# Optimization experiments

Hardware: AMD Instinct MI355X
Metric: run time of the kernel (lower is better)

## Reference

```python
import jax, jax.numpy as jnp
import numpy as np

D = 256  # input_dim
B = 2048

def setup_inputs() -> dict:
    key = jax.random.key(0)
    ks = jax.random.split(key, 6)
    x = jax.random.normal(ks[0], (B, D), dtype=jnp.float32)
    offsets = jax.random.normal(ks[1], (D,), dtype=jnp.float32)
    coeff0 = jax.random.normal(ks[2], (), dtype=jnp.float32)
    coeff1 = jax.random.normal(ks[3], (D,), dtype=jnp.float32)
    coeff2 = jax.random.normal(ks[4], (D, D), dtype=jnp.float32)
    coeff3 = jax.random.normal(ks[5], (D, D, D), dtype=jnp.float32)
    return {"x": x, "offsets": offsets, "coeff0": coeff0, "coeff1": coeff1,
            "coeff2": coeff2, "coeff3": coeff3}

def reference(x, offsets, coeff0, coeff1, coeff2, coeff3):
    # Truncated Taylor series around learned offsets: out[b] = c0 + sum_i <coeff_i, rel^{\otimes i}>[b]
    rel = x - offsets  # (B, D)
    out = coeff0  # scalar, broadcasts to (B,)
    for c in (coeff1, coeff2, coeff3):
        # contract one mode of the rank-i coefficient with rel at a time
        t = jnp.einsum('...d,bd->b...', c, rel)  # (B, D^{i-1})
        while t.ndim > 1:
            t = jnp.einsum('b...d,bd->b...', t, rel)
        out = out + t  # (B,)
    return out
```

## Files before the change

### kernel.cpp

```cpp
#include <hip/hip_runtime.h>
#include <hip/hip_bf16.h>

#define DD 256
#define BB 2048
#define BM 128
#define BN 32
#define NTILE 512
#define NSTAGE (BB / BN)

typedef __bf16 bf16x8 __attribute__((ext_vector_type(8)));
typedef float  f32x4  __attribute__((ext_vector_type(4)));

#define AS1 __attribute__((address_space(1)))
#define AS3 __attribute__((address_space(3)))

__device__ __forceinline__ unsigned short f2bf(float f) {
    unsigned int u = __float_as_uint(f);
    return (unsigned short)((u + 0x7FFFu + ((u >> 16) & 1u)) >> 16);
}
__device__ __forceinline__ float bf2f(unsigned short s) {
    return __uint_as_float(((unsigned int)s) << 16);
}
__device__ __forceinline__ void async_cp16(const void* g, void* l) {
    __builtin_amdgcn_global_load_lds((const AS1 unsigned int*)g,
                                     (AS3 unsigned int*)l, 16, 0, 0);
}

__global__ void prep_all(const float* __restrict__ x, const float* __restrict__ offsets,
                         const float* __restrict__ c0, const float* __restrict__ c1,
                         unsigned short* __restrict__ rel_bf16, float* __restrict__ out) {
    const int tid = threadIdx.x, wave = tid >> 6, lane = tid & 63;
    const float4 o4  = *(const float4*)(offsets + lane * 4);
    const float4 c14 = *(const float4*)(c1 + lane * 4);
#pragma unroll
    for (int i = 0; i < 2; ++i) {
        const int b = blockIdx.x * 8 + wave * 2 + i;
        const float4 x4 = *(const float4*)(x + (size_t)b * DD + lane * 4);
        float4 r;
        r.x = x4.x - o4.x; r.y = x4.y - o4.y; r.z = x4.z - o4.z; r.w = x4.w - o4.w;
        ushort4 rb;
        rb.x = f2bf(r.x); rb.y = f2bf(r.y); rb.z = f2bf(r.z); rb.w = f2bf(r.w);
        *(ushort4*)(rel_bf16 + (size_t)b * DD + lane * 4) = rb;
        float s = r.x * c14.x + r.y * c14.y + r.z * c14.z + r.w * c14.w;
        s += __shfl_xor(s, 1);  s += __shfl_xor(s, 2);  s += __shfl_xor(s, 4);
        s += __shfl_xor(s, 8);  s += __shfl_xor(s, 16); s += __shfl_xor(s, 32);
        if (lane == 0) out[b] = c0[0] + s;
    }
}

__global__ __launch_bounds__(512, 4) void taylor3(
    const float* __restrict__ c3, const float* __restrict__ c2,
    const unsigned short* __restrict__ rel_bf16, float* __restrict__ partial)
{
    __shared__ unsigned short Bs[2][BN * DD];
    __shared__ unsigned short relIbf[BB];
    __shared__ __align__(16) float c2row[BM];
    __shared__ float colsum[2][8][BN];

    const int bidx  = blockIdx.x;
    const int i_t   = bidx >> 1;
    const int jbase = (bidx & 1) << 7;
    const int tid  = threadIdx.x;
    const int wave = tid >> 6;
    const int lane = tid & 63;
    const int wm = wave & 1, wk = wave >> 1;
    const int lrow = lane & 15, quad = lane >> 4;

#pragma unroll
    for (int k = 0; k < 4; ++k) {
        const int b = tid + k * 512;
        relIbf[b] = rel_bf16[(size_t)b * DD + i_t];
    }
    if (tid < BM) c2row[tid] = c2[i_t * DD + jbase + tid];

    bf16x8 afr[2][4];
    {
#pragma unroll
        for (int mt = 0; mt < 4; ++mt) {
            const int j = jbase + wm * 64 + mt * 16 + lrow;
            const float* p = c3 + ((size_t)i_t * DD + j) * DD + wk * 64 + quad * 8;
#pragma unroll
            for (int ks = 0; ks < 2; ++ks) {
                const float4 f0 = *(const float4*)(p + ks * 32);
                const float4 f1 = *(const float4*)(p + ks * 32 + 4);
                union { unsigned short u[8]; bf16x8 v; } cv;
                cv.u[0] = f2bf(f0.x); cv.u[1] = f2bf(f0.y);
                cv.u[2] = f2bf(f0.z); cv.u[3] = f2bf(f0.w);
                cv.u[4] = f2bf(f1.x); cv.u[5] = f2bf(f1.y);
                cv.u[6] = f2bf(f1.z); cv.u[7] = f2bf(f1.w);
                afr[ks][mt] = cv.v;
            }
        }
    }

    auto stage = [&](int nb, int buf) {
        const int b0 = nb * BN;
#pragma unroll
        for (int c = 0; c < 2; ++c) {
            const int r0 = c * 16 + wave * 2;
            const int row = r0 + (lane >> 5);
            const int g = (lane & 31) ^ (row & 7);
            const unsigned short* src = rel_bf16 + (size_t)(b0 + row) * DD + g * 8;
            async_cp16(src, &Bs[buf][r0 * DD]);
        }
    };

    auto body = [&](int nb, int cur) {
        const int b0 = nb * BN;
        __syncthreads();
        if (nb + 1 < NSTAGE) stage(nb + 1, cur ^ 1);

        if (nb > 0 && wave == 0 && lane < BN) {
            const int pb0 = b0 - BN;
            float v = colsum[cur ^ 1][0][lane];
#pragma unroll
            for (int w = 1; w < 8; ++w) v += colsum[cur ^ 1][w][lane];
            partial[(size_t)bidx * BB + pb0 + lane] = bf2f(relIbf[pb0 + lane]) * v;
        }

        f32x4 acc[4][2];
        __builtin_amdgcn_s_setprio(1);
        {
            bf16x8 bfr[2];
#pragma unroll
            for (int nt = 0; nt < 2; ++nt) {
                const int col = nt * 16 + lrow;
                const int glog = wk * 8 + quad;
                const int g = glog ^ (col & 7);
                bfr[nt] = *(const bf16x8*)(&Bs[cur][col * DD + g * 8]);
            }
            const f32x4 z4 = (f32x4){0.f, 0.f, 0.f, 0.f};
#pragma unroll
            for (int mt = 0; mt < 4; ++mt)
#pragma unroll
                for (int nt = 0; nt < 2; ++nt)
                    acc[mt][nt] = __builtin_amdgcn_mfma_f32_16x16x32_bf16(
                        afr[0][mt], bfr[nt], z4, 0, 0, 0);
        }
        {
            bf16x8 bfr[2];
#pragma unroll
            for (int nt = 0; nt < 2; ++nt) {
                const int col = nt * 16 + lrow;
                const int glog = wk * 8 + 4 + quad;
                const int g = glog ^ (col & 7);
                bfr[nt] = *(const bf16x8*)(&Bs[cur][col * DD + g * 8]);
            }
#pragma unroll
            for (int mt = 0; mt < 4; ++mt)
#pragma unroll
                for (int nt = 0; nt < 2; ++nt)
                    acc[mt][nt] = __builtin_amdgcn_mfma_f32_16x16x32_bf16(
                        afr[1][mt], bfr[nt], acc[mt][nt], 0, 0, 0);
        }
        __builtin_amdgcn_s_setprio(0);

        float sv[2];
#pragma unroll
        for (int nt = 0; nt < 2; ++nt) {
            const int col = nt * 16 + lrow;
            float s0 = 0.f, s1 = 0.f;
#pragma unroll
            for (int mt = 0; mt < 4; ++mt) {
                const int el = wm * 64 + mt * 16 + quad * 4;
                const int e  = jbase + el;
                const int g  = (e >> 3) ^ (col & 7);
                const ushort4 rj = *(const ushort4*)(&Bs[cur][col * DD + g * 8 + (e & 7)]);
                f32x4 a = acc[mt][nt];
                if (wk == 0) {
                    const float4 c2r = *(const float4*)(&c2row[el]);
                    a[0] += c2r.x; a[1] += c2r.y; a[2] += c2r.z; a[3] += c2r.w;
                }
                float& sa = (mt & 1) ? s1 : s0;
                sa = fmaf(a[0], bf2f(rj.x), sa);
                sa = fmaf(a[1], bf2f(rj.y), sa);
                sa = fmaf(a[2], bf2f(rj.z), sa);
                sa = fmaf(a[3], bf2f(rj.w), sa);
            }
            float s = s0 + s1;
            s += __shfl_xor(s, 16, 64);
            s += __shfl_xor(s, 32, 64);
            sv[nt] = s;
        }
        if (lane < 32)
            colsum[cur][wave][lane] = (lane & 16) ? sv[1] : sv[0];
    };

    stage(0, 0);
    for (int nb = 0; nb < NSTAGE; nb += 2) {
        body(nb, 0);
        body(nb + 1, 1);
    }

    __syncthreads();
    if (wave == 0 && lane < BN) {
        const int pb0 = BB - BN;
        float v = colsum[1][0][lane];
#pragma unroll
        for (int w = 1; w < 8; ++w) v += colsum[1][w][lane];
        partial[(size_t)bidx * BB + pb0 + lane] = bf2f(relIbf[pb0 + lane]) * v;
    }
}

__global__ void reduce_partial(const float* __restrict__ partial, float* __restrict__ out) {
    __shared__ f32x4 red[256];
    const int t = threadIdx.x;
    const int g = blockIdx.x * 4 + (t & 3);
    const int slice = t >> 2;
    f32x4 s = (f32x4){0.f, 0.f, 0.f, 0.f};
    for (int r = slice * 8; r < slice * 8 + 8; ++r)
        s += *(const f32x4*)(partial + (size_t)r * BB + g * 4);
    red[t] = s; __syncthreads();
    if (t < 128) red[t] += red[t + 128]; __syncthreads();
    if (t < 64)  red[t] += red[t + 64];  __syncthreads();
    if (t < 32)  red[t] += red[t + 32];  __syncthreads();
    if (t < 16)  red[t] += red[t + 16];  __syncthreads();
    if (t < 8)   red[t] += red[t + 8];   __syncthreads();
    if (t < 4) {
        const f32x4 v = red[t] + red[t + 4];
        float4* op = (float4*)(out + (size_t)(blockIdx.x * 4 + t) * 4);
        float4 o = *op;
        o.x += v[0]; o.y += v[1]; o.z += v[2]; o.w += v[3];
        *op = o;
    }
}

extern "C" void kernel_launch(void* const* d_in, const int* in_sizes, int n_in,
                              void* d_out, int out_size, void* d_ws, size_t ws_size,
                              hipStream_t stream) {
    const float* x       = (const float*)d_in[0];
    const float* offsets = (const float*)d_in[1];
    const float* c0      = (const float*)d_in[2];
    const float* c1      = (const float*)d_in[3];
    const float* c2      = (const float*)d_in[4];
    const float* c3      = (const float*)d_in[5];
    float* out = (float*)d_out;

    char* ws = (char*)d_ws;
    unsigned short* rel_bf16 = (unsigned short*)ws;
    float* partial = (float*)(ws + (size_t)1 * 1024 * 1024);

    prep_all<<<BB / 8, 256, 0, stream>>>(x, offsets, c0, c1, rel_bf16, out);
    taylor3<<<NTILE, 512, 0, stream>>>(c3, c2, rel_bf16, partial);
    reduce_partial<<<128, 256, 0, stream>>>(partial, out);
}
```

Baseline: 196.5 us.

## Deepen rel staging to four LDS buffers with explicit vmcnt waits

Changes the shared-memory staging of rel tiles from double buffering to a four-buffer ring, issuing three stages ahead and starting the prefetch before the c3 fragment load. The full __syncthreads at each step becomes a manual s_waitcnt vmcnt plus s_barrier, so outstanding loads can stay in flight across iterations. The aim is to hide global-to-LDS latency more fully. In exchange, LDS use roughly doubles for Bs, which may cut occupancy under the 512-thread, 4-block launch bound. The hand-counted vmcnt values must also match the compiler's actual load counts (including the c3 register loads), or correctness is at risk.

```diff
diff --git a/kernel.cpp b/kernel.cpp
--- a/kernel.cpp
+++ b/kernel.cpp
@@ -7,6 +7,7 @@
 #define BN 32
 #define NTILE 512
 #define NSTAGE (BB / BN)
+#define NBUF 4
 
 typedef __bf16 bf16x8 __attribute__((ext_vector_type(8)));
 typedef float  f32x4  __attribute__((ext_vector_type(4)));
@@ -52,7 +53,7 @@
     const float* __restrict__ c3, const float* __restrict__ c2,
     const unsigned short* __restrict__ rel_bf16, float* __restrict__ partial)
 {
-    __shared__ unsigned short Bs[2][BN * DD];
+    __shared__ unsigned short Bs[NBUF][BN * DD];
     __shared__ unsigned short relIbf[BB];
     __shared__ __align__(16) float c2row[BM];
     __shared__ float colsum[2][8][BN];
@@ -72,6 +73,22 @@
         relIbf[b] = rel_bf16[(size_t)b * DD + i_t];
     }
     if (tid < BM) c2row[tid] = c2[i_t * DD + jbase + tid];
+
+    __syncthreads();
+
+    auto stage = [&](int nb, int buf) {
+        const int b0 = nb * BN;
+#pragma unroll
+        for (int c = 0; c < 2; ++c) {
+            const int r0 = c * 16 + wave * 2;
+            const int row = r0 + (lane >> 5);
+            const int g = (lane & 31) ^ (row & 7);
+            const unsigned short* src = rel_bf16 + (size_t)(b0 + row) * DD + g * 8;
+            async_cp16(src, &Bs[buf][r0 * DD]);
+        }
+    };
+
+    stage(0, 0); stage(1, 1); stage(2, 2);
 
     bf16x8 afr[2][4];
     {
@@ -93,28 +110,19 @@
         }
     }
 
-    auto stage = [&](int nb, int buf) {
-        const int b0 = nb * BN;
-#pragma unroll
-        for (int c = 0; c < 2; ++c) {
-            const int r0 = c * 16 + wave * 2;
-            const int row = r0 + (lane >> 5);
-            const int g = (lane & 31) ^ (row & 7);
-            const unsigned short* src = rel_bf16 + (size_t)(b0 + row) * DD + g * 8;
-            async_cp16(src, &Bs[buf][r0 * DD]);
-        }
-    };
-
-    auto body = [&](int nb, int cur) {
-        const int b0 = nb * BN;
-        __syncthreads();
-        if (nb + 1 < NSTAGE) stage(nb + 1, cur ^ 1);
+    auto body = [&](int nb, int cur, int vm) {
+        if (vm == 4)      asm volatile("s_waitcnt vmcnt(4)" ::: "memory");
+        else if (vm == 2) asm volatile("s_waitcnt vmcnt(2)" ::: "memory");
+        else              asm volatile("s_waitcnt vmcnt(0)" ::: "memory");
+        __builtin_amdgcn_s_barrier();
+
+        if (nb + 3 < NSTAGE) stage(nb + 3, (cur + 3) & 3);
 
         if (nb > 0 && wave == 0 && lane < BN) {
-            const int pb0 = b0 - BN;
-            float v = colsum[cur ^ 1][0][lane];
-#pragma unroll
-            for (int w = 1; w < 8; ++w) v += colsum[cur ^ 1][w][lane];
+            const int pb0 = nb * BN - BN;
+            float v = colsum[(nb - 1) & 1][0][lane];
+#pragma unroll
+            for (int w = 1; w < 8; ++w) v += colsum[(nb - 1) & 1][w][lane];
             partial[(size_t)bidx * BB + pb0 + lane] = bf2f(relIbf[pb0 + lane]) * v;
         }
 
@@ -183,14 +191,19 @@
             sv[nt] = s;
         }
         if (lane < 32)
-            colsum[cur][wave][lane] = (lane & 16) ? sv[1] : sv[0];
+            colsum[nb & 1][wave][lane] = (lane & 16) ? sv[1] : sv[0];
     };
 
-    stage(0, 0);
-    for (int nb = 0; nb < NSTAGE; nb += 2) {
-        body(nb, 0);
-        body(nb + 1, 1);
-    }
+    for (int t = 0; t < 60; t += 4) {
+        body(t,     0, 4);
+        body(t + 1, 1, 4);
+        body(t + 2, 2, 4);
+        body(t + 3, 3, 4);
+    }
+    body(60, 0, 4);
+    body(61, 1, 4);
+    body(62, 2, 2);
+    body(63, 3, 0);
 
     __syncthreads();
     if (wave == 0 && lane < BN) {
```

New measurement: 197.1 us. Within noise of the previous version (+0.3%).
